# Kernel optimization log

Hardware: AMD Instinct MI355X
Metric: run time of the kernel (lower is better)

Reference implementation:

```python
import jax, jax.numpy as jnp
import numpy as np

TAU = 0.5
EPS = 1e-12  # F.normalize default eps


def _projection(z, fc1_w, fc1_b, fc2_w, fc2_b):
    h = jax.nn.elu(z @ fc1_w.T + fc1_b)
    return h @ fc2_w.T + fc2_b


def _normalize(z):
    n = jnp.linalg.norm(z, axis=1, keepdims=True)
    return z / jnp.maximum(n, EPS)


def _semi_loss(h1, h2):
    z1 = _normalize(h1)
    z2 = _normalize(h2)
    refl_sim = jnp.exp((z1 @ z1.T) / TAU)      # [N, N]
    between_sim = jnp.exp((z1 @ z2.T) / TAU)   # [N, N]
    pos = jnp.diagonal(between_sim)
    denom = refl_sim.sum(axis=1) + between_sim.sum(axis=1) - jnp.diagonal(refl_sim)
    return -jnp.log(pos / denom)


def setup_inputs() -> dict:
    key = jax.random.key(0)
    k1, k2, k3, k4 = jax.random.split(key, 4)
    N, H, P = 8192, 512, 512
    s1 = 1.0 / np.sqrt(H)
    s2 = 1.0 / np.sqrt(P)
    return {
        "z1": jax.random.normal(k1, (N, H), jnp.float32),
        "z2": jax.random.normal(k2, (N, H), jnp.float32),
        "fc1_w": jax.random.normal(k3, (P, H), jnp.float32) * s1,
        "fc1_b": jnp.zeros((P,), jnp.float32),
        "fc2_w": jax.random.normal(k4, (H, P), jnp.float32) * s2,
        "fc2_b": jnp.zeros((H,), jnp.float32),
    }


def reference(z1, z2, fc1_w, fc1_b, fc2_w, fc2_b):
    h1 = _projection(z1, fc1_w, fc1_b, fc2_w, fc2_b)
    h2 = _projection(z2, fc1_w, fc1_b, fc2_w, fc2_b)
    l1 = _semi_loss(h1, h2)
    l2 = _semi_loss(h2, h1)
    ret = (l1 + l2) * 0.5
    return ret.mean()
```

## Files before the change

kernel.cpp:

```cpp
#include <hip/hip_runtime.h>
#include <math.h>

typedef __attribute__((ext_vector_type(8))) __bf16 bf16x8;
typedef __attribute__((ext_vector_type(4))) float f32x4;
typedef __attribute__((ext_vector_type(16))) float f32x16;
typedef __attribute__((ext_vector_type(8))) unsigned short u16x8;
typedef __attribute__((ext_vector_type(8))) int i32x8;

#define GAS(p) ((const __attribute__((address_space(1))) void*)(p))
#define LAS(p) ((__attribute__((address_space(3))) void*)(p))

__device__ __forceinline__ unsigned short f2bf(float f) {
  union { float f; unsigned int u; } v; v.f = f;
  unsigned int r = (v.u + 0x7FFFu + ((v.u >> 16) & 1u)) >> 16;
  return (unsigned short)r;
}
__device__ __forceinline__ float bf2f(unsigned short b) {
  union { unsigned int u; float f; } v; v.u = ((unsigned int)b) << 16;
  return v.f;
}

__global__ __launch_bounds__(256) void cast_all_kernel(
    const float* __restrict__ z1, const float* __restrict__ z2,
    const float* __restrict__ w1, const float* __restrict__ w2,
    unsigned short* __restrict__ z1b, unsigned short* __restrict__ z2b,
    unsigned short* __restrict__ w1b, unsigned short* __restrict__ w2b) {
  int b = blockIdx.x;
  const float* in; unsigned short* out; int base;
  if (b < 4096)       { in = z1; out = z1b; base = b; }
  else if (b < 8192)  { in = z2; out = z2b; base = b - 4096; }
  else if (b < 8448)  { in = w1; out = w1b; base = b - 8192; }
  else                { in = w2; out = w2b; base = b - 8448; }
  int i = (base * 256 + threadIdx.x) * 4;
  float4 v = *(const float4*)(in + i);
  ushort4 o;
  o.x = f2bf(v.x); o.y = f2bf(v.y); o.z = f2bf(v.z); o.w = f2bf(v.w);
  *(ushort4*)(out + i) = o;
}

template<int EPI>
__global__ __launch_bounds__(256, 4)
void proj_kernel(const unsigned short* __restrict__ A1,
                 const unsigned short* __restrict__ A2,
                 const unsigned short* __restrict__ W,
                 const float* __restrict__ bias,
                 unsigned short* __restrict__ C1,
                 unsigned short* __restrict__ C2) {
  __shared__ unsigned short lA[2][4096];
  __shared__ unsigned short lB[2][4096];
  const int b = blockIdx.x;
  const int which = b >> 9;
  const int r = b & 511;
  const int m0 = (r >> 3) * 64;
  const int n0 = (r & 7) * 64;
  const unsigned short* A = which ? A2 : A1;
  unsigned short* C = which ? C2 : C1;

  const int tid  = threadIdx.x;
  const int wv   = tid >> 6;
  const int lane = tid & 63;
  const int half = lane >> 5;
  const int l31  = lane & 31;

  const int srow0 = wv * 8 + (lane >> 3);
  const int srow1 = srow0 + 32;
  const int sc0 = ((lane & 7) * 16) ^ ((srow0 & 7) << 4);
  const int sc1 = ((lane & 7) * 16) ^ ((srow1 & 7) << 4);
  const int sdst0 = wv * 1024 + lane * 16;
  const int sdst1 = sdst0 + 4096;

  const char* Ac = (const char*)A;
  const char* Wc = (const char*)W;

#define PROJ_STAGE(buf, kc)                                                    \
  do {                                                                         \
    const size_t kb = (size_t)(kc) * 128;                                      \
    __builtin_amdgcn_global_load_lds(                                          \
        GAS(Ac + (size_t)(m0 + srow0) * 1024 + kb + sc0),                      \
        LAS((char*)&lA[buf][0] + sdst0), 16, 0, 0);                            \
    __builtin_amdgcn_global_load_lds(                                          \
        GAS(Ac + (size_t)(m0 + srow1) * 1024 + kb + sc1),                      \
        LAS((char*)&lA[buf][0] + sdst1), 16, 0, 0);                            \
    __builtin_amdgcn_global_load_lds(                                          \
        GAS(Wc + (size_t)(n0 + srow0) * 1024 + kb + sc0),                      \
        LAS((char*)&lB[buf][0] + sdst0), 16, 0, 0);                            \
    __builtin_amdgcn_global_load_lds(                                          \
        GAS(Wc + (size_t)(n0 + srow1) * 1024 + kb + sc1),                      \
        LAS((char*)&lB[buf][0] + sdst1), 16, 0, 0);                            \
  } while (0)

  const int arow = (wv & 1) * 32 + l31;
  const int brow = (wv >> 1) * 32 + l31;
  const int aoff = arow * 128;
  const int boff = brow * 128;
  const int aswz = (arow & 7) << 4;
  const int bswz = (brow & 7) << 4;

  f32x16 acc;
#pragma unroll
  for (int i = 0; i < 16; ++i) acc[i] = 0.f;

  PROJ_STAGE(0, 0);
  __syncthreads();

  for (int kc = 0; kc < 8; ++kc) {
    if (kc < 7) PROJ_STAGE((kc + 1) & 1, kc + 1);
    const char* bufA = (const char*)&lA[kc & 1][0];
    const char* bufB = (const char*)&lB[kc & 1][0];
#pragma unroll
    for (int s = 0; s < 4; ++s) {
      const int cb = s * 32 + half * 16;
      bf16x8 av = *(const bf16x8*)(bufA + aoff + (cb ^ aswz));
      bf16x8 bv = *(const bf16x8*)(bufB + boff + (cb ^ bswz));
      acc = __builtin_amdgcn_mfma_f32_32x32x16_bf16(av, bv, acc, 0, 0, 0);
    }
    __syncthreads();
  }
#undef PROJ_STAGE

  const int col = n0 + brow;
  const float bvs = bias[col];
#pragma unroll
  for (int reg = 0; reg < 16; ++reg) {
    const int row = m0 + (wv & 1) * 32 + (reg & 3) + 8 * (reg >> 2) + 4 * half;
    float v = acc[reg] + bvs;
    if constexpr (EPI == 0) v = (v > 0.f) ? v : expm1f(v);
    C[(size_t)row * 512 + col] = f2bf(v);
  }
}

__global__ __launch_bounds__(256, 2)
void gram_kernel(const unsigned char* __restrict__ q1,
                 const unsigned char* __restrict__ q2,
                 float* __restrict__ d11, float* __restrict__ d22,
                 float* __restrict__ d12r, float* __restrict__ d12c) {
  __shared__ unsigned char lA[65536];

  const int b = blockIdx.x;
  const unsigned char *Abase, *Bbase;
  float *rptr, *cptr;
  int by, g, cnt;
  bool cross;
  if (b < 2048) {
    const bool first = (b < 1024);
    const int j = first ? b : b - 1024;
    g = j & 15; by = j >> 4;
    cnt = min(4, by + 1 - g * 4);
    if (cnt <= 0) return;
    const unsigned char* h = first ? q1 : q2;
    Abase = h; Bbase = h;
    rptr = first ? d11 : d22; cptr = rptr;
    cross = false;
  } else {
    const int j = b - 2048;
    g = j & 15; by = j >> 4;
    Abase = q1; Bbase = q2;
    rptr = d12r; cptr = d12c;
    cnt = 4; cross = true;
  }

  const int tid  = threadIdx.x;
  const int wave = tid >> 6;
  const int lane = tid & 63;
  const int half = lane >> 5;
  const int l31  = lane & 31;
  const int pa0 = (wave & 1) * 2;
  const int pb0 = (wave >> 1) * 2;
  const int lfo = half * 1024 + l31 * 16;

  {
    const unsigned char* Asrc = Abase + (size_t)(by * 4 + wave) * 16384 + lane * 16;
    unsigned char* Adst = lA + wave * 16384 + lane * 16;
#pragma unroll
    for (int i = 0; i < 16; ++i)
      __builtin_amdgcn_global_load_lds(GAS(Asrc + i * 1024),
                                       LAS(Adst + i * 1024), 16, 0, 0);
  }
  __syncthreads();

  union frag { i32x8 v; int4 h[2]; };

  float rs[2][16];
#pragma unroll
  for (int mi = 0; mi < 2; ++mi)
#pragma unroll
    for (int rr = 0; rr < 16; ++rr) rs[mi][rr] = 0.f;

  for (int t = 0; t < cnt; ++t) {
    const int ct = g * 4 + t;
    const unsigned char* B0 = Bbase + (size_t)(ct * 4 + pb0) * 16384 + lfo;
    const unsigned char* B1 = B0 + 16384;

    f32x16 acc[2][2];
#pragma unroll
    for (int i = 0; i < 2; ++i)
#pragma unroll
      for (int jj = 0; jj < 2; ++jj)
#pragma unroll
        for (int rr = 0; rr < 16; ++rr) acc[i][jj][rr] = 0.f;

#pragma unroll
    for (int KT = 0; KT < 4; ++KT) {
#pragma unroll
      for (int ktl = 0; ktl < 2; ++ktl) {
        const int ko = KT * 4096 + ktl * 2048;
        frag fa[2], fb[2];
        fb[0].h[0] = *(const int4*)(B0 + ko);
        fb[0].h[1] = *(const int4*)(B0 + ko + 512);
        fb[1].h[0] = *(const int4*)(B1 + ko);
        fb[1].h[1] = *(const int4*)(B1 + ko + 512);
#pragma unroll
        for (int i = 0; i < 2; ++i) {
          const int oa = (pa0 + i) * 16384 + ko + lfo;
          fa[i].h[0] = *(const int4*)&lA[oa];
          fa[i].h[1] = *(const int4*)&lA[oa + 512];
        }
#pragma unroll
        for (int mi = 0; mi < 2; ++mi)
#pragma unroll
          for (int ni = 0; ni < 2; ++ni)
            acc[mi][ni] = __builtin_amdgcn_mfma_scale_f32_32x32x64_f8f6f4(
                fa[mi].v, fb[ni].v, acc[mi][ni],
                0, 0,
                0, 0x7F7F7F7F,
                0, 0x7F7F7F7F);
      }
    }

    float cs[2] = {0.f, 0.f};
#pragma unroll
    for (int mi = 0; mi < 2; ++mi)
#pragma unroll
      for (int ni = 0; ni < 2; ++ni)
#pragma unroll
        for (int rr = 0; rr < 16; ++rr) {
          float v = exp2f(2.8853900817779268f * acc[mi][ni][rr]);
          rs[mi][rr] += v;
          cs[ni] += v;
        }
    const bool diag = (!cross) && (ct == by);
    if (!diag) {
#pragma unroll
      for (int ni = 0; ni < 2; ++ni) {
        float v = cs[ni] + __shfl_xor(cs[ni], 32, 64);
        if (half == 0)
          atomicAdd(&cptr[ct * 128 + (wave >> 1) * 64 + ni * 32 + l31], v);
      }
    }
  }

#pragma unroll
  for (int mi = 0; mi < 2; ++mi) {
#pragma unroll
    for (int dd = 1; dd < 32; dd <<= 1) {
#pragma unroll
      for (int rr = 0; rr < 16; ++rr) rs[mi][rr] += __shfl_xor(rs[mi][rr], dd, 64);
    }
    if (l31 == 0) {
      const int mb = by * 128 + (wave & 1) * 64 + mi * 32;
#pragma unroll
      for (int rr = 0; rr < 16; ++rr) {
        const int row = mb + (rr & 3) + 8 * (rr >> 2) + 4 * half;
        atomicAdd(&rptr[row], rs[mi][rr]);
      }
    }
  }
}

__global__ __launch_bounds__(256)
void norm_diag_kernel(const unsigned short* __restrict__ h1,
                      const unsigned short* __restrict__ h2,
                      unsigned char* __restrict__ q1,
                      unsigned char* __restrict__ q2,
                      float* __restrict__ cdiag) {
  const int wave = threadIdx.x >> 6, lane = threadIdx.x & 63;
  const int row = blockIdx.x * 4 + wave;
  const u16x8 u1 = *(const u16x8*)(h1 + (size_t)row * 512 + lane * 8);
  const u16x8 u2 = *(const u16x8*)(h2 + (size_t)row * 512 + lane * 8);
  float f1[8], f2[8], ss1 = 0.f, ss2 = 0.f;
#pragma unroll
  for (int j = 0; j < 8; ++j) {
    f1[j] = bf2f(u1[j]); ss1 += f1[j] * f1[j];
    f2[j] = bf2f(u2[j]); ss2 += f2[j] * f2[j];
  }
#pragma unroll
  for (int d = 1; d < 64; d <<= 1) {
    ss1 += __shfl_xor(ss1, d, 64);
    ss2 += __shfl_xor(ss2, d, 64);
  }
  const float inv1 = 1.0f / fmaxf(sqrtf(ss1), 1e-12f);
  const float inv2 = 1.0f / fmaxf(sqrtf(ss2), 1e-12f);
  float a[8], bb[8];
  float dot = 0.f;
#pragma unroll
  for (int j = 0; j < 8; ++j) {
    a[j] = f1[j] * inv1; bb[j] = f2[j] * inv2;
    dot += a[j] * bb[j];
  }
  int lo1 = __builtin_amdgcn_cvt_pk_fp8_f32(a[0], a[1], 0, false);
  lo1 = __builtin_amdgcn_cvt_pk_fp8_f32(a[2], a[3], lo1, true);
  int hi1 = __builtin_amdgcn_cvt_pk_fp8_f32(a[4], a[5], 0, false);
  hi1 = __builtin_amdgcn_cvt_pk_fp8_f32(a[6], a[7], hi1, true);
  int lo2 = __builtin_amdgcn_cvt_pk_fp8_f32(bb[0], bb[1], 0, false);
  lo2 = __builtin_amdgcn_cvt_pk_fp8_f32(bb[2], bb[3], lo2, true);
  int hi2 = __builtin_amdgcn_cvt_pk_fp8_f32(bb[4], bb[5], 0, false);
  hi2 = __builtin_amdgcn_cvt_pk_fp8_f32(bb[6], bb[7], hi2, true);

  const int c0 = lane * 8;
  const size_t dst = (size_t)(row >> 5) * 16384 + (c0 >> 6) * 2048
                   + ((c0 >> 4) & 3) * 512 + (row & 31) * 16 + (c0 & 15);
  *(int2*)(q1 + dst) = make_int2(lo1, hi1);
  *(int2*)(q2 + dst) = make_int2(lo2, hi2);
#pragma unroll
  for (int d = 1; d < 64; d <<= 1) dot += __shfl_xor(dot, d, 64);
  if (lane == 0) cdiag[row] = dot;
}

__global__ __launch_bounds__(256)
void finalize_kernel(const float* __restrict__ d11, const float* __restrict__ d22,
                     const float* __restrict__ d12r, const float* __restrict__ d12c,
                     const float* __restrict__ cdiag, float* __restrict__ out) {
  const float e2 = 7.38905609893065f;
  float s = 0.f;
  for (int i = threadIdx.x; i < 8192; i += 256) {
    const float den1 = d11[i] + d12r[i] - e2;
    const float den2 = d22[i] + d12c[i] - e2;
    s += -2.0f * cdiag[i] + 0.5f * (logf(den1) + logf(den2));
  }
#pragma unroll
  for (int d = 1; d < 64; d <<= 1) s += __shfl_xor(s, d, 64);
  __shared__ float sm[4];
  if ((threadIdx.x & 63) == 0) sm[threadIdx.x >> 6] = s;
  __syncthreads();
  if (threadIdx.x == 0) out[0] = (sm[0] + sm[1] + sm[2] + sm[3]) * (1.0f / 8192.0f);
}

extern "C" void kernel_launch(void* const* d_in, const int* in_sizes, int n_in,
                              void* d_out, int out_size, void* d_ws, size_t ws_size,
                              hipStream_t stream) {
  const float* z1 = (const float*)d_in[0];
  const float* z2 = (const float*)d_in[1];
  const float* w1 = (const float*)d_in[2];
  const float* b1 = (const float*)d_in[3];
  const float* w2 = (const float*)d_in[4];
  const float* b2 = (const float*)d_in[5];
  float* out = (float*)d_out;

  const int N = 8192, D = 512;
  char* ws = (char*)d_ws;
  auto alloc = [&](size_t bytes) {
    char* p = ws; ws += (bytes + 255) & ~(size_t)255; return p;
  };
  unsigned short* z1b = (unsigned short*)alloc((size_t)N * D * 2);
  unsigned short* z2b = (unsigned short*)alloc((size_t)N * D * 2);
  unsigned short* g1  = (unsigned short*)alloc((size_t)N * D * 2);
  unsigned short* g2  = (unsigned short*)alloc((size_t)N * D * 2);
  unsigned short* w1b = (unsigned short*)alloc((size_t)D * D * 2);
  unsigned short* w2b = (unsigned short*)alloc((size_t)D * D * 2);
  float* sums  = (float*)alloc((size_t)4 * N * sizeof(float));
  float* cdiag = (float*)alloc((size_t)N * sizeof(float));
  float* d11 = sums, *d22 = sums + N, *d12r = sums + 2 * N, *d12c = sums + 3 * N;
  unsigned short* h1 = z1b;
  unsigned short* h2 = z2b;
  unsigned char* q1 = (unsigned char*)g1;
  unsigned char* q2 = (unsigned char*)g2;

  hipMemsetAsync(sums, 0, (size_t)4 * N * sizeof(float), stream);

  cast_all_kernel<<<dim3(8704), 256, 0, stream>>>(z1, z2, w1, w2, z1b, z2b, w1b, w2b);
  proj_kernel<0><<<dim3(1024), 256, 0, stream>>>(z1b, z2b, w1b, b1, g1, g2);
  proj_kernel<1><<<dim3(1024), 256, 0, stream>>>(g1, g2, w2b, b2, h1, h2);
  norm_diag_kernel<<<dim3(N / 4), 256, 0, stream>>>(h1, h2, q1, q2, cdiag);
  gram_kernel<<<dim3(3072), 256, 0, stream>>>(q1, q2, d11, d22, d12r, d12c);
  finalize_kernel<<<1, 256, 0, stream>>>(d11, d22, d12r, d12c, cdiag, out);
}
```

Measured before the change: 266.6 us.

## Pre-swizzle weights for direct MFMA loads and compact triangular gram grid

After: 244.7 us. 8.2% less time.

```diff
diff --git a/kernel.cpp b/kernel.cpp
--- a/kernel.cpp
+++ b/kernel.cpp
@@ -26,28 +26,39 @@
     unsigned short* __restrict__ z1b, unsigned short* __restrict__ z2b,
     unsigned short* __restrict__ w1b, unsigned short* __restrict__ w2b) {
   int b = blockIdx.x;
-  const float* in; unsigned short* out; int base;
-  if (b < 4096)       { in = z1; out = z1b; base = b; }
-  else if (b < 8192)  { in = z2; out = z2b; base = b - 4096; }
-  else if (b < 8448)  { in = w1; out = w1b; base = b - 8192; }
-  else                { in = w2; out = w2b; base = b - 8448; }
-  int i = (base * 256 + threadIdx.x) * 4;
-  float4 v = *(const float4*)(in + i);
-  ushort4 o;
-  o.x = f2bf(v.x); o.y = f2bf(v.y); o.z = f2bf(v.z); o.w = f2bf(v.w);
-  *(ushort4*)(out + i) = o;
+  if (b < 8192) {
+    const float* in = (b < 4096) ? z1 : z2;
+    unsigned short* out = (b < 4096) ? z1b : z2b;
+    int base = (b < 4096) ? b : b - 4096;
+    int i = (base * 256 + threadIdx.x) * 4;
+    float4 v = *(const float4*)(in + i);
+    ushort4 o;
+    o.x = f2bf(v.x); o.y = f2bf(v.y); o.z = f2bf(v.z); o.w = f2bf(v.w);
+    *(ushort4*)(out + i) = o;
+  } else {
+    const float* in = (b < 8448) ? w1 : w2;
+    unsigned short* out = (b < 8448) ? w1b : w2b;
+    int base = (b < 8448) ? b - 8192 : b - 8448;
+    int i = (base * 256 + threadIdx.x) * 4;
+    float4 v = *(const float4*)(in + i);
+    unsigned int lo = (unsigned)f2bf(v.x) | ((unsigned)f2bf(v.y) << 16);
+    unsigned int hi = (unsigned)f2bf(v.z) | ((unsigned)f2bf(v.w) << 16);
+    const int col = i >> 9, k = i & 511;
+    const size_t dst = (size_t)(col >> 5) * 32768 + (size_t)(k >> 4) * 1024
+                     + (size_t)((k >> 3) & 1) * 512 + (col & 31) * 16 + (k & 7) * 2;
+    *(int2*)((char*)out + dst) = make_int2((int)lo, (int)hi);
+  }
 }
 
 template<int EPI>
 __global__ __launch_bounds__(256, 4)
 void proj_kernel(const unsigned short* __restrict__ A1,
                  const unsigned short* __restrict__ A2,
-                 const unsigned short* __restrict__ W,
+                 const unsigned short* __restrict__ Wf,
                  const float* __restrict__ bias,
                  unsigned short* __restrict__ C1,
                  unsigned short* __restrict__ C2) {
   __shared__ unsigned short lA[2][4096];
-  __shared__ unsigned short lB[2][4096];
   const int b = blockIdx.x;
   const int which = b >> 9;
   const int r = b & 511;
@@ -68,9 +79,7 @@
   const int sc1 = ((lane & 7) * 16) ^ ((srow1 & 7) << 4);
   const int sdst0 = wv * 1024 + lane * 16;
   const int sdst1 = sdst0 + 4096;
-
   const char* Ac = (const char*)A;
-  const char* Wc = (const char*)W;
 
 #define PROJ_STAGE(buf, kc)                                                    \
   do {                                                                         \
@@ -81,20 +90,14 @@
     __builtin_amdgcn_global_load_lds(                                          \
         GAS(Ac + (size_t)(m0 + srow1) * 1024 + kb + sc1),                      \
         LAS((char*)&lA[buf][0] + sdst1), 16, 0, 0);                            \
-    __builtin_amdgcn_global_load_lds(                                          \
-        GAS(Wc + (size_t)(n0 + srow0) * 1024 + kb + sc0),                      \
-        LAS((char*)&lB[buf][0] + sdst0), 16, 0, 0);                            \
-    __builtin_amdgcn_global_load_lds(                                          \
-        GAS(Wc + (size_t)(n0 + srow1) * 1024 + kb + sc1),                      \
-        LAS((char*)&lB[buf][0] + sdst1), 16, 0, 0);                            \
   } while (0)
 
   const int arow = (wv & 1) * 32 + l31;
-  const int brow = (wv >> 1) * 32 + l31;
   const int aoff = arow * 128;
-  const int boff = brow * 128;
   const int aswz = (arow & 7) << 4;
-  const int bswz = (brow & 7) << 4;
+  const char* Wb = (const char*)Wf
+                 + (size_t)((n0 >> 5) + (wv >> 1)) * 32768
+                 + half * 512 + l31 * 16;
 
   f32x16 acc;
 #pragma unroll
@@ -106,19 +109,17 @@
   for (int kc = 0; kc < 8; ++kc) {
     if (kc < 7) PROJ_STAGE((kc + 1) & 1, kc + 1);
     const char* bufA = (const char*)&lA[kc & 1][0];
-    const char* bufB = (const char*)&lB[kc & 1][0];
 #pragma unroll
     for (int s = 0; s < 4; ++s) {
-      const int cb = s * 32 + half * 16;
-      bf16x8 av = *(const bf16x8*)(bufA + aoff + (cb ^ aswz));
-      bf16x8 bv = *(const bf16x8*)(bufB + boff + (cb ^ bswz));
+      bf16x8 av = *(const bf16x8*)(bufA + aoff + ((s * 32 + half * 16) ^ aswz));
+      bf16x8 bv = *(const bf16x8*)(Wb + (size_t)(kc * 4 + s) * 1024);
       acc = __builtin_amdgcn_mfma_f32_32x32x16_bf16(av, bv, acc, 0, 0, 0);
     }
     __syncthreads();
   }
 #undef PROJ_STAGE
 
-  const int col = n0 + brow;
+  const int col = n0 + (wv >> 1) * 32 + l31;
   const float bvs = bias[col];
 #pragma unroll
   for (int reg = 0; reg < 16; ++reg) {
@@ -141,19 +142,24 @@
   float *rptr, *cptr;
   int by, g, cnt;
   bool cross;
-  if (b < 2048) {
-    const bool first = (b < 1024);
-    const int j = first ? b : b - 1024;
-    g = j & 15; by = j >> 4;
-    cnt = min(4, by + 1 - g * 4);
-    if (cnt <= 0) return;
+  if (b < 1088) {
+    const bool first = (b < 544);
+    int j = first ? b : b - 544;
+    int q = (int)((sqrtf(2.f * j + 1.f) - 1.f) * 0.5f);
+    while (2 * (q + 1) * (q + 2) <= j) ++q;
+    while (2 * q * (q + 1) > j) --q;
+    const int w = j - 2 * q * (q + 1);
+    const int dr = w / (q + 1);
+    g = w - dr * (q + 1);
+    by = 4 * q + dr;
     const unsigned char* h = first ? q1 : q2;
     Abase = h; Bbase = h;
     rptr = first ? d11 : d22; cptr = rptr;
+    cnt = min(4, by + 1 - g * 4);
     cross = false;
   } else {
-    const int j = b - 2048;
-    g = j & 15; by = j >> 4;
+    const int j = b - 1088;
+    g = j >> 6; by = j & 63;
     Abase = q1; Bbase = q2;
     rptr = d12r; cptr = d12c;
     cnt = 4; cross = true;
@@ -371,6 +377,6 @@
   proj_kernel<0><<<dim3(1024), 256, 0, stream>>>(z1b, z2b, w1b, b1, g1, g2);
   proj_kernel<1><<<dim3(1024), 256, 0, stream>>>(g1, g2, w2b, b2, h1, h2);
   norm_diag_kernel<<<dim3(N / 4), 256, 0, stream>>>(h1, h2, q1, q2, cdiag);
-  gram_kernel<<<dim3(3072), 256, 0, stream>>>(q1, q2, d11, d22, d12r, d12c);
+  gram_kernel<<<dim3(2112), 256, 0, stream>>>(q1, q2, d11, d22, d12r, d12c);
   finalize_kernel<<<1, 256, 0, stream>>>(d11, d22, d12r, d12c, cdiag, out);
 }
```
